# Kernel tuning notes

Hardware: AMD Instinct MI355X
Metric: run time of the kernel (lower is better)

## Reference

```python
import jax, jax.numpy as jnp
import numpy as np

N, D, K = 32768, 128, 16
EPS = 1e-8  # torch cosine_similarity eps


def setup_inputs() -> dict:
    key = jax.random.key(0)
    k1, k2, kW1, kW2, kV = jax.random.split(key, 5)
    # xavier_normal std for [K, fan_in, fan_out]-style tensors (torch treats dim0 as batch? no:
    # xavier_normal_ on a 3D tensor uses fan_in = D*1? torch computes fan from dims 1.. with receptive field.
    # fan_in = size(1)*rf, fan_out = size(0)*rf where rf = prod(shape[2:]).
    def xavier_std(shape):
        rf = int(np.prod(shape[2:])) if len(shape) > 2 else 1
        fan_in = shape[1] * rf
        fan_out = shape[0] * rf
        return float(np.sqrt(2.0 / (fan_in + fan_out)))
    W1 = jax.random.normal(kW1, (K, D, D), jnp.float32) * xavier_std((K, D, D))
    W2 = jax.random.normal(kW2, (K, D, D), jnp.float32) * xavier_std((K, D, D))
    V = jax.random.normal(kV, (K, 2 * D, 1), jnp.float32) * xavier_std((K, 2 * D, 1))
    b = jnp.zeros((K,), jnp.float32)
    x_1 = jax.random.normal(k1, (N, D), jnp.float32)
    x_2 = jax.random.normal(k2, (N, D), jnp.float32)
    return {"x_1": x_1, "x_2": x_2, "W1": W1, "W2": W2, "V": V, "b": b}


def reference(x_1, x_2, W1, W2, V, b):
    # Batched version of the per-slice loop: one bmm per side instead of K matmuls.
    x1_t = jnp.einsum('nd,kde->kne', x_1, W1)  # [K, N, D]
    x2_t = jnp.einsum('nd,kde->kne', x_2, W2)  # [K, N, D]
    # torch.cosine_similarity(dim=-1): dot / (clamp(||a||, eps) * clamp(||b||, eps))
    num = jnp.sum(x1_t * x2_t, axis=-1)                      # [K, N]
    n1 = jnp.maximum(jnp.sqrt(jnp.sum(x1_t * x1_t, -1)), EPS)
    n2 = jnp.maximum(jnp.sqrt(jnp.sum(x2_t * x2_t, -1)), EPS)
    part1 = num / (n1 * n2)                                  # [K, N]
    x_cat = jnp.concatenate([x_1, x_2], axis=-1)             # [N, 2D]
    part2 = jnp.einsum('nc,kc->kn', x_cat, V[:, :, 0])       # [K, N]
    fea = part1 + part2 + b[:, None]                         # [K, N]
    return jax.nn.relu(fea.T)                                # [N, K]
```

## Files before the change

kernel.cpp:

```cpp
#include <hip/hip_runtime.h>


typedef __attribute__((ext_vector_type(8))) __bf16 bf16x8;
typedef __attribute__((ext_vector_type(8))) unsigned short us8;
typedef __attribute__((ext_vector_type(4))) float f32x4;

static __device__ __forceinline__ unsigned short f2bf(float f) {
  unsigned u = __float_as_uint(f);
  u += 0x7FFFu + ((u >> 16) & 1u);
  return (unsigned short)(u >> 16);
}

static __device__ __forceinline__ bf16x8 as_bf(us8 u) {
  bf16x8 r;
  __builtin_memcpy(&r, &u, sizeof(r));
  return r;
}

__global__ void ntn_prep(const float* __restrict__ W1, const float* __restrict__ W2,
                         const float* __restrict__ V,
                         unsigned short* __restrict__ wsW, unsigned short* __restrict__ wsV) {
  int t = blockIdx.x * 256 + threadIdx.x;
  if (t < 65536) {
    int u = t & 2047;
    int lane = u & 63, s = (u >> 6) & 3, et = (u >> 8) & 7;
    int cc = t >> 11, side = cc & 1, k = cc >> 1;
    int q = lane >> 4, l15 = lane & 15;
    const float* W = side ? W2 : W1;
    const float* src = W + k * 16384 + (s * 32 + q * 8) * 128 + (et * 16 + l15);
    us8 r;
#pragma unroll
    for (int j = 0; j < 8; ++j) r[j] = f2bf(src[j * 128]);
    *(us8*)(wsW + (size_t)t * 8) = r;
  } else if (t < 66048) {
    int u = t - 65536;
    int lane = u & 63, cs = u >> 6;
    int q = lane >> 4, l15 = lane & 15;
    const float* src = V + l15 * 256 + cs * 32 + q * 8;
    us8 r;
#pragma unroll
    for (int j = 0; j < 8; ++j) r[j] = f2bf(src[j]);
    *(us8*)(wsV + (size_t)u * 8) = r;
  }
}

__global__ __launch_bounds__(256, 1) void ntn_main(
    const float* __restrict__ x1, const float* __restrict__ x2,
    const float* __restrict__ b,
    const unsigned short* __restrict__ wsW, const unsigned short* __restrict__ wsV,
    float* __restrict__ out) {
  __shared__ uint4 ldsW[2][2048];

  const int tid = threadIdx.x;
  const int lane = tid & 63, wave = tid >> 6;
  const int q = lane >> 4, l15 = lane & 15;
  const int rowbase = blockIdx.x * 128 + wave * 32;

  const f32x4 zero4 = {0.f, 0.f, 0.f, 0.f};

  bf16x8 xb[2][2][4];
#pragma unroll
  for (int side = 0; side < 2; ++side) {
    const float* xp0 = side ? x2 : x1;
#pragma unroll
    for (int nt = 0; nt < 2; ++nt) {
#pragma unroll
      for (int s = 0; s < 4; ++s) {
        const float* p = xp0 + (size_t)(rowbase + nt * 16 + l15) * 128 + s * 32 + q * 8;
        float4 v0 = *(const float4*)p;
        float4 v1 = *(const float4*)(p + 4);
        us8 uu;
        uu[0] = f2bf(v0.x); uu[1] = f2bf(v0.y); uu[2] = f2bf(v0.z); uu[3] = f2bf(v0.w);
        uu[4] = f2bf(v1.x); uu[5] = f2bf(v1.y); uu[6] = f2bf(v1.z); uu[7] = f2bf(v1.w);
        xb[side][nt][s] = as_bf(uu);
      }
    }
  }

  auto stage = [&](int cc, int slot) {
    const unsigned short* src = wsW + (size_t)cc * 16384 + (size_t)(wave * 512 + lane) * 8;
    uint4* dst = &ldsW[slot][wave * 512];
#pragma unroll
    for (int i = 0; i < 8; ++i)
      __builtin_amdgcn_global_load_lds(
          (__attribute__((address_space(1))) void*)(void*)(src + i * 512),
          (__attribute__((address_space(3))) void*)(dst + i * 64), 16, 0, 0);
  };

  stage(0, 0);

  {
    bf16x8 vf[8];
#pragma unroll
    for (int cs = 0; cs < 8; ++cs)
      vf[cs] = as_bf(*(const us8*)(wsV + (size_t)(cs * 64 + lane) * 8));
    float4 bv = *(const float4*)(b + q * 4);
#pragma unroll
    for (int nt = 0; nt < 2; ++nt) {
      f32x4 accP = zero4;
#pragma unroll
      for (int cs = 0; cs < 8; ++cs)
        accP = __builtin_amdgcn_mfma_f32_16x16x32_bf16(vf[cs], xb[cs >> 2][nt][cs & 3], accP, 0, 0, 0);
      accP.x += bv.x; accP.y += bv.y; accP.z += bv.z; accP.w += bv.w;
      int row = rowbase + nt * 16 + l15;
      *(f32x4*)(out + (size_t)row * 16 + q * 4) = accP;
    }
  }

  f32x4 acc1[8][2];
#pragma unroll 1
  for (int k = 0; k < 16; ++k) {
    __syncthreads();
    stage(2 * k + 1, 1);
#pragma unroll
    for (int et = 0; et < 8; ++et) {
      bf16x8 wa[4];
#pragma unroll
      for (int s = 0; s < 4; ++s)
        wa[s] = as_bf(*(const us8*)&ldsW[0][(et * 4 + s) * 64 + lane]);
#pragma unroll
      for (int nt = 0; nt < 2; ++nt) {
        f32x4 a = zero4;
#pragma unroll
        for (int s = 0; s < 4; ++s)
          a = __builtin_amdgcn_mfma_f32_16x16x32_bf16(wa[s], xb[0][nt][s], a, 0, 0, 0);
        acc1[et][nt] = a;
      }
    }
    __syncthreads();
    if (k < 15) stage(2 * k + 2, 0);

    float nm[2] = {0.f, 0.f}, q1[2] = {0.f, 0.f}, q2[2] = {0.f, 0.f};
#pragma unroll
    for (int et = 0; et < 8; ++et) {
      bf16x8 wb[4];
#pragma unroll
      for (int s = 0; s < 4; ++s)
        wb[s] = as_bf(*(const us8*)&ldsW[1][(et * 4 + s) * 64 + lane]);
#pragma unroll
      for (int nt = 0; nt < 2; ++nt) {
        f32x4 a2 = zero4;
#pragma unroll
        for (int s = 0; s < 4; ++s)
          a2 = __builtin_amdgcn_mfma_f32_16x16x32_bf16(wb[s], xb[1][nt][s], a2, 0, 0, 0);
        f32x4 a1 = acc1[et][nt];
        nm[nt] += a1.x * a2.x + a1.y * a2.y + a1.z * a2.z + a1.w * a2.w;
        q1[nt] += a1.x * a1.x + a1.y * a1.y + a1.z * a1.z + a1.w * a1.w;
        q2[nt] += a2.x * a2.x + a2.y * a2.y + a2.z * a2.z + a2.w * a2.w;
      }
    }
#pragma unroll
    for (int nt = 0; nt < 2; ++nt) {
      nm[nt] += __shfl_xor(nm[nt], 16); nm[nt] += __shfl_xor(nm[nt], 32);
      q1[nt] += __shfl_xor(q1[nt], 16); q1[nt] += __shfl_xor(q1[nt], 32);
      q2[nt] += __shfl_xor(q2[nt], 16); q2[nt] += __shfl_xor(q2[nt], 32);
      float n1 = fmaxf(sqrtf(q1[nt]), 1e-8f);
      float n2 = fmaxf(sqrtf(q2[nt]), 1e-8f);
      float p1 = nm[nt] / (n1 * n2);
      if (lane < 16) {
        float* po = out + (size_t)(rowbase + nt * 16 + lane) * 16 + k;
        *po = fmaxf(p1 + *po, 0.f);
      }
    }
  }
}

extern "C" void kernel_launch(void* const* d_in, const int* in_sizes, int n_in,
                              void* d_out, int out_size, void* d_ws, size_t ws_size,
                              hipStream_t stream) {
  const float* x1 = (const float*)d_in[0];
  const float* x2 = (const float*)d_in[1];
  const float* W1 = (const float*)d_in[2];
  const float* W2 = (const float*)d_in[3];
  const float* V  = (const float*)d_in[4];
  const float* b  = (const float*)d_in[5];
  float* out = (float*)d_out;
  unsigned short* wsW = (unsigned short*)d_ws;
  unsigned short* wsV = wsW + (size_t)65536 * 8;

  ntn_prep<<<258, 256, 0, stream>>>(W1, W2, V, wsW, wsV);
  ntn_main<<<256, 256, 0, stream>>>(x1, x2, b, wsW, wsV, out);
}
```

Before: 131.3 us.

## Split K slices across blocks, stage half-W1/half-W2 chunks, raise occupancy

The main kernel now launches 512 blocks. Each block handles 256 rows and a quarter of the K slices (4 slices), instead of 128 rows and all 16. Prep repacks W so that each 16K-element chunk holds half of a slice's W1 and half of its W2. Both sides are then computed together from one LDS buffer, with no acc1 storage held across the two halves. Launch bounds allow 2 blocks per CU, and the part2 result stays in registers rather than being re-read from the output. In exchange, x rows are loaded and converted to bf16 four times across blocks, and each wave holds twice as many x fragments in registers.

```diff
diff --git a/kernel.cpp b/kernel.cpp
--- a/kernel.cpp
+++ b/kernel.cpp
@@ -23,9 +23,10 @@
   int t = blockIdx.x * 256 + threadIdx.x;
   if (t < 65536) {
     int u = t & 2047;
-    int lane = u & 63, s = (u >> 6) & 3, et = (u >> 8) & 7;
-    int cc = t >> 11, side = cc & 1, k = cc >> 1;
+    int lane = u & 63, s = (u >> 6) & 3, et2 = (u >> 8) & 3, side = (u >> 10) & 1;
+    int cc = t >> 11, h = cc & 1, k = cc >> 1;
     int q = lane >> 4, l15 = lane & 15;
+    int et = h * 4 + et2;
     const float* W = side ? W2 : W1;
     const float* src = W + k * 16384 + (s * 32 + q * 8) * 128 + (et * 16 + l15);
     us8 r;
@@ -44,7 +45,7 @@
   }
 }
 
-__global__ __launch_bounds__(256, 1) void ntn_main(
+__global__ __launch_bounds__(256, 2) void ntn_main(
     const float* __restrict__ x1, const float* __restrict__ x2,
     const float* __restrict__ b,
     const unsigned short* __restrict__ wsW, const unsigned short* __restrict__ wsV,
@@ -54,16 +55,30 @@
   const int tid = threadIdx.x;
   const int lane = tid & 63, wave = tid >> 6;
   const int q = lane >> 4, l15 = lane & 15;
-  const int rowbase = blockIdx.x * 128 + wave * 32;
+  const int kh = blockIdx.x & 3;
+  const int rb = blockIdx.x >> 2;
+  const int rowbase = rb * 256 + wave * 64;
 
   const f32x4 zero4 = {0.f, 0.f, 0.f, 0.f};
 
-  bf16x8 xb[2][2][4];
+  auto stage = [&](int cc, int slot) {
+    const unsigned short* src = wsW + (size_t)cc * 16384 + (size_t)(wave * 512 + lane) * 8;
+    uint4* dst = &ldsW[slot][wave * 512];
+#pragma unroll
+    for (int i = 0; i < 8; ++i)
+      __builtin_amdgcn_global_load_lds(
+          (__attribute__((address_space(1))) void*)(void*)(src + i * 512),
+          (__attribute__((address_space(3))) void*)(dst + i * 64), 16, 0, 0);
+  };
+
+  stage(kh * 8 + 0, 0);
+
+  bf16x8 xb[2][4][4];
 #pragma unroll
   for (int side = 0; side < 2; ++side) {
     const float* xp0 = side ? x2 : x1;
 #pragma unroll
-    for (int nt = 0; nt < 2; ++nt) {
+    for (int nt = 0; nt < 4; ++nt) {
 #pragma unroll
       for (int s = 0; s < 4; ++s) {
         const float* p = xp0 + (size_t)(rowbase + nt * 16 + l15) * 128 + s * 32 + q * 8;
@@ -77,18 +92,7 @@
     }
   }
 
-  auto stage = [&](int cc, int slot) {
-    const unsigned short* src = wsW + (size_t)cc * 16384 + (size_t)(wave * 512 + lane) * 8;
-    uint4* dst = &ldsW[slot][wave * 512];
-#pragma unroll
-    for (int i = 0; i < 8; ++i)
-      __builtin_amdgcn_global_load_lds(
-          (__attribute__((address_space(1))) void*)(void*)(src + i * 512),
-          (__attribute__((address_space(3))) void*)(dst + i * 64), 16, 0, 0);
-  };
-
-  stage(0, 0);
-
+  f32x4 accP[4];
   {
     bf16x8 vf[8];
 #pragma unroll
@@ -96,71 +100,70 @@
       vf[cs] = as_bf(*(const us8*)(wsV + (size_t)(cs * 64 + lane) * 8));
     float4 bv = *(const float4*)(b + q * 4);
 #pragma unroll
-    for (int nt = 0; nt < 2; ++nt) {
-      f32x4 accP = zero4;
+    for (int nt = 0; nt < 4; ++nt) {
+      f32x4 a = zero4;
 #pragma unroll
       for (int cs = 0; cs < 8; ++cs)
-        accP = __builtin_amdgcn_mfma_f32_16x16x32_bf16(vf[cs], xb[cs >> 2][nt][cs & 3], accP, 0, 0, 0);
-      accP.x += bv.x; accP.y += bv.y; accP.z += bv.z; accP.w += bv.w;
-      int row = rowbase + nt * 16 + l15;
-      *(f32x4*)(out + (size_t)row * 16 + q * 4) = accP;
+        a = __builtin_amdgcn_mfma_f32_16x16x32_bf16(vf[cs], xb[cs >> 2][nt][cs & 3], a, 0, 0, 0);
+      a.x += bv.x; a.y += bv.y; a.z += bv.z; a.w += bv.w;
+      accP[nt] = a;
     }
   }
 
-  f32x4 acc1[8][2];
-#pragma unroll 1
-  for (int k = 0; k < 16; ++k) {
-    __syncthreads();
-    stage(2 * k + 1, 1);
+  float nm[4] = {0.f, 0.f, 0.f, 0.f};
+  float q1[4] = {0.f, 0.f, 0.f, 0.f};
+  float q2[4] = {0.f, 0.f, 0.f, 0.f};
+
+  auto compute = [&](int slot) {
 #pragma unroll
-    for (int et = 0; et < 8; ++et) {
-      bf16x8 wa[4];
+    for (int et = 0; et < 4; ++et) {
+      bf16x8 wa[4], wb[4];
 #pragma unroll
-      for (int s = 0; s < 4; ++s)
-        wa[s] = as_bf(*(const us8*)&ldsW[0][(et * 4 + s) * 64 + lane]);
+      for (int s = 0; s < 4; ++s) {
+        wa[s] = as_bf(*(const us8*)&ldsW[slot][et * 256 + s * 64 + lane]);
+        wb[s] = as_bf(*(const us8*)&ldsW[slot][1024 + et * 256 + s * 64 + lane]);
+      }
 #pragma unroll
-      for (int nt = 0; nt < 2; ++nt) {
-        f32x4 a = zero4;
+      for (int nt = 0; nt < 4; ++nt) {
+        f32x4 a1 = zero4, a2 = zero4;
 #pragma unroll
         for (int s = 0; s < 4; ++s)
-          a = __builtin_amdgcn_mfma_f32_16x16x32_bf16(wa[s], xb[0][nt][s], a, 0, 0, 0);
-        acc1[et][nt] = a;
-      }
-    }
-    __syncthreads();
-    if (k < 15) stage(2 * k + 2, 0);
-
-    float nm[2] = {0.f, 0.f}, q1[2] = {0.f, 0.f}, q2[2] = {0.f, 0.f};
-#pragma unroll
-    for (int et = 0; et < 8; ++et) {
-      bf16x8 wb[4];
-#pragma unroll
-      for (int s = 0; s < 4; ++s)
-        wb[s] = as_bf(*(const us8*)&ldsW[1][(et * 4 + s) * 64 + lane]);
-#pragma unroll
-      for (int nt = 0; nt < 2; ++nt) {
-        f32x4 a2 = zero4;
+          a1 = __builtin_amdgcn_mfma_f32_16x16x32_bf16(wa[s], xb[0][nt][s], a1, 0, 0, 0);
 #pragma unroll
         for (int s = 0; s < 4; ++s)
           a2 = __builtin_amdgcn_mfma_f32_16x16x32_bf16(wb[s], xb[1][nt][s], a2, 0, 0, 0);
-        f32x4 a1 = acc1[et][nt];
         nm[nt] += a1.x * a2.x + a1.y * a2.y + a1.z * a2.z + a1.w * a2.w;
         q1[nt] += a1.x * a1.x + a1.y * a1.y + a1.z * a1.z + a1.w * a1.w;
         q2[nt] += a2.x * a2.x + a2.y * a2.y + a2.z * a2.z + a2.w * a2.w;
       }
     }
+  };
+
+#pragma unroll 1
+  for (int kk = 0; kk < 4; ++kk) {
+    const int cbase = kh * 8 + 2 * kk;
+    __syncthreads();
+    stage(cbase + 1, 1);
+    compute(0);
+    __syncthreads();
+    if (kk < 3) stage(cbase + 2, 0);
+    compute(1);
+
+    const int k = kh * 4 + kk;
 #pragma unroll
-    for (int nt = 0; nt < 2; ++nt) {
-      nm[nt] += __shfl_xor(nm[nt], 16); nm[nt] += __shfl_xor(nm[nt], 32);
-      q1[nt] += __shfl_xor(q1[nt], 16); q1[nt] += __shfl_xor(q1[nt], 32);
-      q2[nt] += __shfl_xor(q2[nt], 16); q2[nt] += __shfl_xor(q2[nt], 32);
-      float n1 = fmaxf(sqrtf(q1[nt]), 1e-8f);
-      float n2 = fmaxf(sqrtf(q2[nt]), 1e-8f);
-      float p1 = nm[nt] / (n1 * n2);
-      if (lane < 16) {
-        float* po = out + (size_t)(rowbase + nt * 16 + lane) * 16 + k;
-        *po = fmaxf(p1 + *po, 0.f);
-      }
+    for (int nt = 0; nt < 4; ++nt) {
+      float n = nm[nt], s1 = q1[nt], s2 = q2[nt];
+      n  += __shfl_xor(n, 16);  n  += __shfl_xor(n, 32);
+      s1 += __shfl_xor(s1, 16); s1 += __shfl_xor(s1, 32);
+      s2 += __shfl_xor(s2, 16); s2 += __shfl_xor(s2, 32);
+      float d1 = fmaxf(sqrtf(s1), 1e-8f);
+      float d2 = fmaxf(sqrtf(s2), 1e-8f);
+      float p1 = n / (d1 * d2);
+      float pc = (kk == 0) ? accP[nt].x : (kk == 1) ? accP[nt].y
+               : (kk == 2) ? accP[nt].z : accP[nt].w;
+      if (q == kh)
+        out[(size_t)(rowbase + nt * 16 + l15) * 16 + k] = fmaxf(p1 + pc, 0.f);
+      nm[nt] = 0.f; q1[nt] = 0.f; q2[nt] = 0.f;
     }
   }
 }
@@ -179,5 +182,5 @@
   unsigned short* wsV = wsW + (size_t)65536 * 8;
 
   ntn_prep<<<258, 256, 0, stream>>>(W1, W2, V, wsW, wsV);
-  ntn_main<<<256, 256, 0, stream>>>(x1, x2, b, wsW, wsV, out);
+  ntn_main<<<512, 256, 0, stream>>>(x1, x2, b, wsW, wsV, out);
 }
```

Result: slower. 268.6 us (+104.5%).
